# Kernel tuning notes

Hardware: AMD Instinct MI355X
Metric: run time of the kernel (lower is better)

## Reference

```python
import jax, jax.numpy as jnp
import numpy as np

D_MODEL = 768
N_HEAD = 12
N_KV_HEADS = 4
HEAD_DIM = D_MODEL // N_HEAD
N_REPEAT = N_HEAD // N_KV_HEADS
ROPE_BASE = 10000.0


def _rotate_half(x):
    # Faithful to the torch impl: reshape(..., 2, d/2) -> transpose(-2,-1) -> reshape
    # (interleaves the two halves), then chunk and cat(-x2, x1).
    d = x.shape[-1]
    xh = x.reshape(*x.shape[:-1], 2, d // 2).swapaxes(-2, -1).reshape(x.shape)
    x1, x2 = jnp.split(xh, 2, axis=-1)
    return jnp.concatenate([-x2, x1], axis=-1)


def _rope(x, pos):
    # x: [B, h, T, d], pos: [T] int
    d = x.shape[-1]
    inv_freq = 1.0 / (ROPE_BASE ** (jnp.arange(0, d, 2, dtype=jnp.float32) / d))
    freqs = pos.astype(jnp.float32)[:, None] * inv_freq[None, :]      # [T, d/2]
    emb = jnp.concatenate([freqs, freqs], axis=-1)                     # [T, d]
    cos = jnp.cos(emb)[None, None]                                     # [1,1,T,d]
    sin = jnp.sin(emb)[None, None]
    xf = x.astype(jnp.float32)
    return (xf * cos + _rotate_half(xf) * sin).astype(x.dtype)


def setup_inputs() -> dict:
    key = jax.random.key(0)
    ks = jax.random.split(key, 6)
    B, T, C = 8, 1024, D_MODEL
    s = 0.02
    return {
        "x": jax.random.normal(ks[0], (B, T, C), dtype=jnp.float32),
        "pos": jnp.arange(T, dtype=jnp.int32),
        "q_w": jax.random.normal(ks[1], (C, N_HEAD * HEAD_DIM), dtype=jnp.float32) * s,
        "q_b": jnp.zeros((N_HEAD * HEAD_DIM,), dtype=jnp.float32),
        "k_w": jax.random.normal(ks[2], (C, N_KV_HEADS * HEAD_DIM), dtype=jnp.float32) * s,
        "k_b": jnp.zeros((N_KV_HEADS * HEAD_DIM,), dtype=jnp.float32),
        "v_w": jax.random.normal(ks[3], (C, N_KV_HEADS * HEAD_DIM), dtype=jnp.float32) * s,
        "v_b": jnp.zeros((N_KV_HEADS * HEAD_DIM,), dtype=jnp.float32),
        "o_w": jax.random.normal(ks[4], (C, C), dtype=jnp.float32) * s,
        "o_b": jnp.zeros((C,), dtype=jnp.float32),
    }


def reference(x, pos, q_w, q_b, k_w, k_b, v_w, v_b, o_w, o_b):
    B, T, C = x.shape
    hd, H, KVH, rep = HEAD_DIM, N_HEAD, N_KV_HEADS, N_REPEAT

    Q = (x @ q_w + q_b).reshape(B, T, H, hd).transpose(0, 2, 1, 3)     # [B,H,T,hd]
    K = (x @ k_w + k_b).reshape(B, T, KVH, hd).transpose(0, 2, 1, 3)   # [B,KVH,T,hd]
    V = (x @ v_w + v_b).reshape(B, T, KVH, hd).transpose(0, 2, 1, 3)

    Q = _rope(Q, pos)
    K = _rope(K, pos)

    # Grouped attention: avoid materializing repeated KV (equiv. to repeat_interleave).
    Qg = Q.reshape(B, KVH, rep, T, hd)
    scores = jnp.einsum("bgrtd,bgsd->bgrts", Qg, K) / np.sqrt(hd).astype(np.float32)
    causal = jnp.tril(jnp.ones((T, T), dtype=bool))
    scores = jnp.where(causal, scores, jnp.finfo(scores.dtype).min)
    probs = jax.nn.softmax(scores, axis=-1)
    out = jnp.einsum("bgrts,bgsd->bgrtd", probs, V)                    # [B,KVH,rep,T,hd]
    out = out.reshape(B, H, T, hd).transpose(0, 2, 1, 3).reshape(B, T, C)
    return out @ o_w + o_b
```

## Files before the change

kernel.cpp:

```cpp
#include <hip/hip_runtime.h>
#include <hip/hip_bf16.h>
#include <math.h>

#define BATCH 8
#define SEQ   1024
#define DM    768
#define NHEAD 12
#define KVH   4
#define HD    64
#define REP   3

#define QSCALE 0.18033688011112042f

typedef unsigned short u16;
typedef __attribute__((ext_vector_type(8))) __bf16 bf16x8;
typedef __attribute__((ext_vector_type(4))) float f32x4;
typedef __attribute__((ext_vector_type(4))) unsigned int u32x4;
typedef __attribute__((address_space(1))) const unsigned int gu32_c;
typedef __attribute__((address_space(3))) unsigned int su32;

__device__ __forceinline__ u16 f2bf(float f) {
    unsigned int u = __float_as_uint(f);
    u += 0x7fffu + ((u >> 16) & 1u);
    return (u16)(u >> 16);
}

__global__ __launch_bounds__(256) void cvt_all(
    const float* __restrict__ x,
    const float* __restrict__ qw, const float* __restrict__ kw,
    const float* __restrict__ vw, const float* __restrict__ ow,
    u16* __restrict__ xb, u16* __restrict__ wqkvt, u16* __restrict__ wot)
{
    const int NX = 8192 * DM / 4;
    const int NW = 1280 * DM;
    const int NO = DM * DM;
    const int i = blockIdx.x * 256 + threadIdx.x;
    if (i < NX) {
        const float4 v = ((const float4*)x)[i];
        ushort4 r;
        r.x = f2bf(v.x); r.y = f2bf(v.y); r.z = f2bf(v.z); r.w = f2bf(v.w);
        ((ushort4*)xb)[i] = r;
    } else if (i < NX + NW) {
        const int idx = i - NX;
        const int k = idx % DM;
        const int n = idx / DM;
        float v;
        if (n < 768)       v = qw[(size_t)k * 768 + n] * QSCALE;
        else if (n < 1024) v = kw[(size_t)k * 256 + (n - 768)];
        else               v = vw[(size_t)k * 256 + (n - 1024)];
        wqkvt[idx] = f2bf(v);
    } else if (i < NX + NW + NO) {
        const int idx = i - NX - NW;
        const int k = idx % DM;
        const int n = idx / DM;
        wot[idx] = f2bf(ow[(size_t)k * DM + n]);
    }
}

__device__ __forceinline__ void gemm128_body(
    const u16* __restrict__ A, const u16* __restrict__ B,
    int m0, int n0, u16 (*As)[4096], u16 (*Bs)[4096], f32x4 acc[4][4])
{
    const int tid  = threadIdx.x;
    const int lane = tid & 63;
    const int wid  = tid >> 6;
    const int wr = wid >> 1, wc = wid & 1;
    const int lo = lane & 15, hi = lane >> 4;

    const f32x4 z = {0.f, 0.f, 0.f, 0.f};
    #pragma unroll
    for (int i = 0; i < 4; i++)
        #pragma unroll
        for (int j = 0; j < 4; j++)
            acc[i][j] = z;

    const int NT = DM / 32;

    #define STAGE_G(kt_, sl_) do {                                            \
        _Pragma("unroll")                                                     \
        for (int r_ = 0; r_ < 2; ++r_) {                                      \
            const int idx_  = r_ * 256 + tid;                                 \
            const int row_  = idx_ >> 2;                                      \
            const int col_  = (idx_ & 3) << 3;                                \
            const int base_ = (r_ * 256 + wid * 64) * 8;                      \
            __builtin_amdgcn_global_load_lds(                                 \
                (gu32_c*)&A[(size_t)(m0 + row_) * DM + (kt_) * 32 + col_],    \
                (su32*)&As[sl_][base_], 16, 0, 0);                            \
            __builtin_amdgcn_global_load_lds(                                 \
                (gu32_c*)&B[(size_t)(n0 + row_) * DM + (kt_) * 32 + col_],    \
                (su32*)&Bs[sl_][base_], 16, 0, 0);                            \
        }                                                                     \
    } while (0)

    STAGE_G(0, 0);
    STAGE_G(1, 1);

    for (int kt = 0; kt < NT; ++kt) {
        const int k2 = (kt + 2 < NT) ? kt + 2 : NT - 1;
        STAGE_G(k2, (kt + 2) & 3);
        asm volatile("s_waitcnt vmcnt(8)" ::: "memory");
        __builtin_amdgcn_s_barrier();
        __builtin_amdgcn_sched_barrier(0);

        const int sl = kt & 3;
        bf16x8 af[4], bfr[4];
        #pragma unroll
        for (int i = 0; i < 4; i++) af[i]  = *(const bf16x8*)&As[sl][(wr * 64 + i * 16 + lo) * 32 + hi * 8];
        #pragma unroll
        for (int j = 0; j < 4; j++) bfr[j] = *(const bf16x8*)&Bs[sl][(wc * 64 + j * 16 + lo) * 32 + hi * 8];
        #pragma unroll
        for (int i = 0; i < 4; i++)
            #pragma unroll
            for (int j = 0; j < 4; j++)
                acc[i][j] = __builtin_amdgcn_mfma_f32_16x16x32_bf16(af[i], bfr[j], acc[i][j], 0, 0, 0);
    }
    #undef STAGE_G
}

__global__ __launch_bounds__(256) void gemm_qkv(
    const u16* __restrict__ xb, const u16* __restrict__ wt,
    const float* __restrict__ qb, const float* __restrict__ kb,
    const float* __restrict__ vb,
    u16* __restrict__ Q, u16* __restrict__ K, u16* __restrict__ Vr)
{
    __shared__ __align__(16) u16 As[4][4096];
    __shared__ __align__(16) u16 Bs[4][4096];
    const int id = (blockIdx.x & 7) * 80 + (blockIdx.x >> 3);
    const int m0 = (id / 10) * 128;
    const int n0 = (id % 10) * 128;
    f32x4 acc[4][4];
    gemm128_body(xb, wt, m0, n0, As, Bs, acc);

    const int tid = threadIdx.x;
    const int lane = tid & 63, wid = tid >> 6;
    const int wr = wid >> 1, wc = wid & 1;
    const int lo = lane & 15, hi = lane >> 4;

    #pragma unroll
    for (int j = 0; j < 4; j++) {
        const int n = n0 + wc * 64 + j * 16 + lo;
        u16* outp; int nl, Hcnt; float bias;
        if (n < 768)       { outp = Q;  nl = n;        Hcnt = NHEAD; bias = qb[n] * QSCALE; }
        else if (n < 1024) { outp = K;  nl = n - 768;  Hcnt = KVH;   bias = kb[nl]; }
        else               { outp = Vr; nl = n - 1024; Hcnt = KVH;   bias = vb[nl]; }
        const int head = nl >> 6, d = nl & 63;
        #pragma unroll
        for (int i = 0; i < 4; i++) {
            #pragma unroll
            for (int r = 0; r < 4; r++) {
                const int m = m0 + wr * 64 + i * 16 + hi * 4 + r;
                const int b = m >> 10, t = m & 1023;
                outp[(((size_t)(b * Hcnt + head)) * SEQ + t) * HD + d] =
                    f2bf(acc[i][j][r] + bias);
            }
        }
    }
}

__global__ __launch_bounds__(256) void vtrans_k(
    const u16* __restrict__ in, u16* __restrict__ out)
{
    __shared__ u16 T[64][72];
    const int blk = blockIdx.x;
    const int bg  = blk >> 4;
    const int t0  = (blk & 15) << 6;
    const int tid = threadIdx.x;
    const int tl  = tid & 63;
    const int d0  = (tid >> 6) << 4;

    union { u32x4 v[2]; u16 u[16]; } ld;
    const u16* src = in + ((size_t)bg * SEQ + t0 + tl) * HD + d0;
    ld.v[0] = *(const u32x4*)(src);
    ld.v[1] = *(const u32x4*)(src + 8);
    #pragma unroll
    for (int k = 0; k < 16; ++k) T[d0 + k][tl] = ld.u[k];
    __syncthreads();

    const int d  = tid >> 2;
    const int tc = (tid & 3) << 4;
    u16* dst = out + ((size_t)bg * HD + d) * SEQ + t0 + tc;
    *(u32x4*)(dst)     = *(const u32x4*)&T[d][tc];
    *(u32x4*)(dst + 8) = *(const u32x4*)&T[d][tc + 8];
}

__global__ __launch_bounds__(256) void gemm_oproj(
    const u16* __restrict__ Ab, const u16* __restrict__ wt,
    const float* __restrict__ ob, float* __restrict__ outp)
{
    __shared__ __align__(16) u16 As[4][4096];
    __shared__ __align__(16) u16 Bs[4][4096];
    const int id = (blockIdx.x & 7) * 48 + (blockIdx.x >> 3);
    const int m0 = (id / 6) * 128;
    const int n0 = (id % 6) * 128;
    f32x4 acc[4][4];
    gemm128_body(Ab, wt, m0, n0, As, Bs, acc);

    const int tid = threadIdx.x;
    const int lane = tid & 63, wid = tid >> 6;
    const int wr = wid >> 1, wc = wid & 1;
    const int lo = lane & 15, hi = lane >> 4;

    #pragma unroll
    for (int j = 0; j < 4; j++) {
        const int n = n0 + wc * 64 + j * 16 + lo;
        const float bias = ob[n];
        #pragma unroll
        for (int i = 0; i < 4; i++) {
            #pragma unroll
            for (int r = 0; r < 4; r++) {
                const int m = m0 + wr * 64 + i * 16 + hi * 4 + r;
                outp[(size_t)m * DM + n] = acc[i][j][r] + bias;
            }
        }
    }
}

__global__ __launch_bounds__(256) void rope_naive(
    const __hip_bfloat16* __restrict__ Qin, __hip_bfloat16* __restrict__ Qout,
    const __hip_bfloat16* __restrict__ Kin, __hip_bfloat16* __restrict__ Kout,
    const int* __restrict__ pos)
{
    const long long qrows = (long long)BATCH * NHEAD * SEQ;
    const long long krows = (long long)BATCH * KVH * SEQ;
    const long long gid = (long long)blockIdx.x * 256 + threadIdx.x;
    if (gid >= (qrows + krows) * 64) return;
    long long row = gid >> 6;
    const int j = (int)(gid & 63);
    const __hip_bfloat16* in; __hip_bfloat16* outb;
    if (row < qrows) { in = Qin; outb = Qout; }
    else             { in = Kin; outb = Kout; row -= qrows; }
    const int t = (int)(row & (SEQ - 1));

    float p;
    if (pos[1] == 1)                              p = (float)pos[t];
    else if (((const float*)pos)[1] == 1.0f)      p = ((const float*)pos)[t];
    else                                          p = (float)pos[2 * t];

    const float inv = exp2f(-(float)(j & 31) * (13.287712379549449f / 32.0f));
    float sv, cv;
    sincosf(p * inv, &sv, &cv);
    const int partner = (j & 1) * 32 + (j >> 1) + ((j < 32) ? 16 : -16);
    const float sign  = (j < 32) ? -1.0f : 1.0f;
    const float val  = __bfloat162float(in[row * HD + j]);
    const float pv   = __bfloat162float(in[row * HD + partner]);
    outb[row * HD + j] = __float2bfloat16(val * cv + sign * pv * sv);
}

__device__ __forceinline__ void strip_compute(
    const bf16x8& qf0, const bf16x8& qf1,
    const bf16x8& k0, const bf16x8& k1, const bf16x8& k2, const bf16x8& k3,
    const bf16x8* vv, bool diag, int msk0, int hi,
    float& m, float& l, f32x4* O)
{
    const f32x4 z = {0.f, 0.f, 0.f, 0.f};
    f32x4 a0 = z, a1 = z;
    __builtin_amdgcn_s_setprio(1);
    a0 = __builtin_amdgcn_mfma_f32_16x16x32_bf16(k0, qf0, a0, 0, 0, 0);
    a0 = __builtin_amdgcn_mfma_f32_16x16x32_bf16(k1, qf1, a0, 0, 0, 0);
    a1 = __builtin_amdgcn_mfma_f32_16x16x32_bf16(k2, qf0, a1, 0, 0, 0);
    a1 = __builtin_amdgcn_mfma_f32_16x16x32_bf16(k3, qf1, a1, 0, 0, 0);
    __builtin_amdgcn_s_setprio(0);

    float sc[8];
    #pragma unroll
    for (int e = 0; e < 8; ++e)
        sc[e] = (e < 4) ? a0[e & 3] : a1[e & 3];
    if (diag) {
        #pragma unroll
        for (int e = 0; e < 8; ++e) {
            const int srel = ((e >> 2) << 4) + (hi << 2) + (e & 3);
            if (srel > msk0) sc[e] = -3.0e38f;
        }
    }
    float pm = sc[0];
    #pragma unroll
    for (int e = 1; e < 8; ++e) pm = fmaxf(pm, sc[e]);

    if (!__all(pm - m <= 8.0f)) {
        float pr = fmaxf(pm, __shfl_xor(pm, 16));
        pr = fmaxf(pr, __shfl_xor(pr, 32));
        const float mn = fmaxf(m, pr);
        const float f = exp2f(m - mn);
        l *= f;
        #pragma unroll
        for (int r = 0; r < 4; ++r) {
            const float fr = __shfl(f, hi * 4 + r);
            #pragma unroll
            for (int dj = 0; dj < 4; ++dj) O[dj][r] *= fr;
        }
        m = mn;
    }

    union { u16 u[8]; bf16x8 v; } pu;
    float ps = 0.f;
    #pragma unroll
    for (int e = 0; e < 8; ++e) {
        const float p = exp2f(sc[e] - m);
        ps += p;
        pu.u[e] = f2bf(p);
    }
    l += ps;

    __builtin_amdgcn_s_setprio(1);
    #pragma unroll
    for (int dj = 0; dj < 4; ++dj)
        O[dj] = __builtin_amdgcn_mfma_f32_16x16x32_bf16(pu.v, vv[dj], O[dj], 0, 0, 0);
    __builtin_amdgcn_s_setprio(0);
}

__global__ __launch_bounds__(256, 4) void attn_mfma(
    const u16* __restrict__ Q, const u16* __restrict__ K,
    const u16* __restrict__ Vt, u16* __restrict__ outp)
{
    __shared__ __align__(16) u16 Ks[4][2048];
    __shared__ __align__(16) u16 Vs[4][2048];

    const int blk = blockIdx.x;
    const int xcd = blk & 7;
    const int jj  = blk >> 3;
    const int bg  = (xcd << 2) + (jj & 3);
    const int rh  = jj >> 2;
    const int a   = 15 - rh / 3;
    const int hl  = rh % 3;
    const int b   = bg >> 2, g = bg & 3;
    const int h   = g * REP + hl;

    const int wid  = threadIdx.x >> 6;
    const int lane = threadIdx.x & 63;
    const int lo = lane & 15, hi = lane >> 4;

    const int w    = (a << 2) + wid;
    const int q0   = w << 4;
    const int dT   = w >> 1;
    const int msk0 = lo + ((w & 1) << 4);
    const int nstT = (a << 1) + 2;

    const u16* Kp = K  + (size_t)(b * KVH + g) * SEQ * HD;
    const u16* Vp = Vt + (size_t)(b * KVH + g) * SEQ * HD;

    const int jK = (wid << 6) + lane;
    const int sKoff = (jK ^ ((jK >> 3) & 7)) << 3;
    int vsoff[4];
    #pragma unroll
    for (int q = 0; q < 4; ++q) {
        const int dw  = (wid << 8) + (q << 6) + lane;
        const int R   = dw >> 4;
        const int wd  = dw & 15;
        const int hpl = (wd >> 2) ^ ((R >> 1) & 3);
        vsoff[q] = (R << 10) + (hpl << 2) + (((wd >> 1) & 1) << 4) + ((wd & 1) << 1);
    }

    const u16* Qp = Q + ((size_t)(b * NHEAD + h) * SEQ + q0) * HD;
    const bf16x8 qf0 = *(const bf16x8*)&Qp[(size_t)lo * HD + hi * 8];
    const bf16x8 qf1 = *(const bf16x8*)&Qp[(size_t)lo * HD + 32 + hi * 8];

    const f32x4 z = {0.f, 0.f, 0.f, 0.f};
    f32x4 O[4];
    #pragma unroll
    for (int dj = 0; dj < 4; ++dj) O[dj] = z;
    float m = -3.0e38f, l = 0.f;

    #define STAGE(st_, sl_) do {                                              \
        const int s0_ = (st_) << 5;                                           \
        __builtin_amdgcn_global_load_lds(                                     \
            (gu32_c*)(Kp + (s0_ << 6) + sKoff),                               \
            (su32*)&Ks[sl_][wid << 9], 16, 0, 0);                             \
        _Pragma("unroll")                                                     \
        for (int q_ = 0; q_ < 4; ++q_)                                        \
            __builtin_amdgcn_global_load_lds(                                 \
                (gu32_c*)(Vp + s0_ + vsoff[q_]),                              \
                (su32*)&Vs[sl_][(wid << 9) + (q_ << 7)], 4, 0, 0);            \
    } while (0)

    STAGE(0, 0);
    STAGE(1, 1);

    const int xorK = lo & 7;
    for (int st = 0; st < nstT; ++st) {
        const int s2 = (st + 2 < nstT) ? st + 2 : nstT - 1;
        STAGE(s2, (st + 2) & 3);
        asm volatile("s_waitcnt vmcnt(10)" ::: "memory");
        __builtin_amdgcn_s_barrier();
        __builtin_amdgcn_sched_barrier(0);

        if (st <= dT) {
            const int sl = st & 3;
            const u16* kb_ = Ks[sl];
            const bf16x8 k0 = *(const bf16x8*)&kb_[((lo << 3) + (hi ^ xorK)) << 3];
            const bf16x8 k1 = *(const bf16x8*)&kb_[((lo << 3) + ((4 + hi) ^ xorK)) << 3];
            const bf16x8 k2 = *(const bf16x8*)&kb_[(((16 + lo) << 3) + (hi ^ xorK)) << 3];
            const bf16x8 k3 = *(const bf16x8*)&kb_[(((16 + lo) << 3) + ((4 + hi) ^ xorK)) << 3];
            bf16x8 vv[4];
            #pragma unroll
            for (int dj = 0; dj < 4; ++dj) {
                const int R = dj * 16 + lo;
                vv[dj] = *(const bf16x8*)&Vs[sl][(R << 5) + ((hi ^ ((R >> 1) & 3)) << 3)];
            }
            strip_compute(qf0, qf1, k0, k1, k2, k3, vv, st == dT, msk0, hi, m, l, O);
        }
    }
    #undef STAGE

    l += __shfl_xor(l, 16); l += __shfl_xor(l, 32);
    #pragma unroll
    for (int r = 0; r < 4; ++r) {
        const float li = 1.0f / fmaxf(__shfl(l, hi * 4 + r), 1e-37f);
        const int t = q0 + hi * 4 + r;
        #pragma unroll
        for (int dj = 0; dj < 4; ++dj)
            outp[((size_t)(b * SEQ + t)) * DM + h * HD + dj * 16 + lo] = f2bf(O[dj][r] * li);
    }
}

extern "C" void kernel_launch(void* const* d_in, const int* in_sizes, int n_in,
                              void* d_out, int out_size, void* d_ws, size_t ws_size,
                              hipStream_t stream) {
    const float* x   = (const float*)d_in[0];
    const int*   pos = (const int*)d_in[1];
    const float* qw  = (const float*)d_in[2];
    const float* qb  = (const float*)d_in[3];
    const float* kw  = (const float*)d_in[4];
    const float* kb  = (const float*)d_in[5];
    const float* vw  = (const float*)d_in[6];
    const float* vb  = (const float*)d_in[7];
    const float* ow  = (const float*)d_in[8];
    const float* ob  = (const float*)d_in[9];
    float* out = (float*)d_out;

    u16* xb    = (u16*)d_ws;
    u16* Wqkvt = xb    + (size_t)8192 * DM;
    u16* Wot   = Wqkvt + (size_t)1280 * DM;
    u16* Qbuf  = Wot   + (size_t)DM * DM;
    u16* Kbuf  = Qbuf  + (size_t)BATCH * NHEAD * SEQ * HD;
    u16* Krot  = Kbuf  + (size_t)BATCH * KVH * SEQ * HD;
    u16* Vtb   = Krot  + (size_t)BATCH * KVH * SEQ * HD;
    u16* Qrot  = xb;
    u16* attn  = Qbuf;
    u16* Vraw  = Krot;

    const int NCVT = 8192 * DM / 4 + 1280 * DM + DM * DM;
    cvt_all<<<(NCVT + 255) / 256, 256, 0, stream>>>(x, qw, kw, vw, ow, xb, Wqkvt, Wot);

    gemm_qkv<<<640, 256, 0, stream>>>(xb, Wqkvt, qb, kb, vb, Qbuf, Kbuf, Vraw);

    vtrans_k<<<512, 256, 0, stream>>>(Vraw, Vtb);

    const long long allrows = (long long)BATCH * (NHEAD + KVH) * SEQ;
    rope_naive<<<(int)((allrows * 64 + 255) / 256), 256, 0, stream>>>(
        (const __hip_bfloat16*)Qbuf, (__hip_bfloat16*)Qrot,
        (const __hip_bfloat16*)Kbuf, (__hip_bfloat16*)Krot, pos);

    attn_mfma<<<1536, 256, 0, stream>>>(Qrot, Krot, Vtb, attn);

    gemm_oproj<<<384, 256, 0, stream>>>(attn, Wot, ob, out);
}
```

Before: 215.1 us.

## Shrink GEMM M-tile to 64 and fuse V transpose into QKV epilogue

```diff
diff --git a/kernel.cpp b/kernel.cpp
--- a/kernel.cpp
+++ b/kernel.cpp
@@ -57,9 +57,9 @@
     }
 }
 
-__device__ __forceinline__ void gemm128_body(
+__device__ __forceinline__ void gemm64_body(
     const u16* __restrict__ A, const u16* __restrict__ B,
-    int m0, int n0, u16 (*As)[4096], u16 (*Bs)[4096], f32x4 acc[4][4])
+    int m0, int n0, u16 (*As)[2048], u16 (*Bs)[4096], f32x4 acc[2][4])
 {
     const int tid  = threadIdx.x;
     const int lane = tid & 63;
@@ -69,14 +69,19 @@
 
     const f32x4 z = {0.f, 0.f, 0.f, 0.f};
     #pragma unroll
-    for (int i = 0; i < 4; i++)
+    for (int i = 0; i < 2; i++)
         #pragma unroll
         for (int j = 0; j < 4; j++)
             acc[i][j] = z;
 
     const int NT = DM / 32;
+    const int rowA = tid >> 2;
+    const int colA = (tid & 3) << 3;
 
     #define STAGE_G(kt_, sl_) do {                                            \
+        __builtin_amdgcn_global_load_lds(                                     \
+            (gu32_c*)&A[(size_t)(m0 + rowA) * DM + (kt_) * 32 + colA],        \
+            (su32*)&As[sl_][wid << 9], 16, 0, 0);                             \
         _Pragma("unroll")                                                     \
         for (int r_ = 0; r_ < 2; ++r_) {                                      \
             const int idx_  = r_ * 256 + tid;                                 \
@@ -84,9 +89,6 @@
             const int col_  = (idx_ & 3) << 3;                                \
             const int base_ = (r_ * 256 + wid * 64) * 8;                      \
             __builtin_amdgcn_global_load_lds(                                 \
-                (gu32_c*)&A[(size_t)(m0 + row_) * DM + (kt_) * 32 + col_],    \
-                (su32*)&As[sl_][base_], 16, 0, 0);                            \
-            __builtin_amdgcn_global_load_lds(                                 \
                 (gu32_c*)&B[(size_t)(n0 + row_) * DM + (kt_) * 32 + col_],    \
                 (su32*)&Bs[sl_][base_], 16, 0, 0);                            \
         }                                                                     \
@@ -98,18 +100,18 @@
     for (int kt = 0; kt < NT; ++kt) {
         const int k2 = (kt + 2 < NT) ? kt + 2 : NT - 1;
         STAGE_G(k2, (kt + 2) & 3);
-        asm volatile("s_waitcnt vmcnt(8)" ::: "memory");
+        asm volatile("s_waitcnt vmcnt(6)" ::: "memory");
         __builtin_amdgcn_s_barrier();
         __builtin_amdgcn_sched_barrier(0);
 
         const int sl = kt & 3;
-        bf16x8 af[4], bfr[4];
-        #pragma unroll
-        for (int i = 0; i < 4; i++) af[i]  = *(const bf16x8*)&As[sl][(wr * 64 + i * 16 + lo) * 32 + hi * 8];
+        bf16x8 af[2], bfr[4];
+        #pragma unroll
+        for (int i = 0; i < 2; i++) af[i]  = *(const bf16x8*)&As[sl][(wr * 32 + i * 16 + lo) * 32 + hi * 8];
         #pragma unroll
         for (int j = 0; j < 4; j++) bfr[j] = *(const bf16x8*)&Bs[sl][(wc * 64 + j * 16 + lo) * 32 + hi * 8];
         #pragma unroll
-        for (int i = 0; i < 4; i++)
+        for (int i = 0; i < 2; i++)
             #pragma unroll
             for (int j = 0; j < 4; j++)
                 acc[i][j] = __builtin_amdgcn_mfma_f32_16x16x32_bf16(af[i], bfr[j], acc[i][j], 0, 0, 0);
@@ -117,19 +119,19 @@
     #undef STAGE_G
 }
 
-__global__ __launch_bounds__(256) void gemm_qkv(
+__global__ __launch_bounds__(256, 2) void gemm_qkv(
     const u16* __restrict__ xb, const u16* __restrict__ wt,
     const float* __restrict__ qb, const float* __restrict__ kb,
     const float* __restrict__ vb,
-    u16* __restrict__ Q, u16* __restrict__ K, u16* __restrict__ Vr)
-{
-    __shared__ __align__(16) u16 As[4][4096];
+    u16* __restrict__ Q, u16* __restrict__ K, u16* __restrict__ Vt)
+{
+    __shared__ __align__(16) u16 As[4][2048];
     __shared__ __align__(16) u16 Bs[4][4096];
-    const int id = (blockIdx.x & 7) * 80 + (blockIdx.x >> 3);
-    const int m0 = (id / 10) * 128;
+    const int id = (blockIdx.x & 7) * 160 + (blockIdx.x >> 3);
+    const int m0 = (id / 10) * 64;
     const int n0 = (id % 10) * 128;
-    f32x4 acc[4][4];
-    gemm128_body(xb, wt, m0, n0, As, Bs, acc);
+    f32x4 acc[2][4];
+    gemm64_body(xb, wt, m0, n0, As, Bs, acc);
 
     const int tid = threadIdx.x;
     const int lane = tid & 63, wid = tid >> 6;
@@ -139,61 +141,51 @@
     #pragma unroll
     for (int j = 0; j < 4; j++) {
         const int n = n0 + wc * 64 + j * 16 + lo;
-        u16* outp; int nl, Hcnt; float bias;
-        if (n < 768)       { outp = Q;  nl = n;        Hcnt = NHEAD; bias = qb[n] * QSCALE; }
-        else if (n < 1024) { outp = K;  nl = n - 768;  Hcnt = KVH;   bias = kb[nl]; }
-        else               { outp = Vr; nl = n - 1024; Hcnt = KVH;   bias = vb[nl]; }
-        const int head = nl >> 6, d = nl & 63;
-        #pragma unroll
-        for (int i = 0; i < 4; i++) {
-            #pragma unroll
-            for (int r = 0; r < 4; r++) {
-                const int m = m0 + wr * 64 + i * 16 + hi * 4 + r;
+        if (n < 1024) {
+            u16* outp; int nl, Hcnt; float bias;
+            if (n < 768) { outp = Q; nl = n;       Hcnt = NHEAD; bias = qb[n] * QSCALE; }
+            else         { outp = K; nl = n - 768; Hcnt = KVH;   bias = kb[nl]; }
+            const int head = nl >> 6, d = nl & 63;
+            #pragma unroll
+            for (int i = 0; i < 2; i++) {
+                #pragma unroll
+                for (int r = 0; r < 4; r++) {
+                    const int m = m0 + wr * 32 + i * 16 + hi * 4 + r;
+                    const int b = m >> 10, t = m & 1023;
+                    outp[(((size_t)(b * Hcnt + head)) * SEQ + t) * HD + d] =
+                        f2bf(acc[i][j][r] + bias);
+                }
+            }
+        } else {
+            const int nl = n - 1024;
+            const float bias = vb[nl];
+            const int head = nl >> 6, d = nl & 63;
+            #pragma unroll
+            for (int i = 0; i < 2; i++) {
+                ushort4 vs;
+                vs.x = f2bf(acc[i][j][0] + bias);
+                vs.y = f2bf(acc[i][j][1] + bias);
+                vs.z = f2bf(acc[i][j][2] + bias);
+                vs.w = f2bf(acc[i][j][3] + bias);
+                const int m = m0 + wr * 32 + i * 16 + hi * 4;
                 const int b = m >> 10, t = m & 1023;
-                outp[(((size_t)(b * Hcnt + head)) * SEQ + t) * HD + d] =
-                    f2bf(acc[i][j][r] + bias);
+                *(ushort4*)&Vt[(((size_t)(b * KVH + head)) * HD + d) * SEQ + t] = vs;
             }
         }
     }
 }
 
-__global__ __launch_bounds__(256) void vtrans_k(
-    const u16* __restrict__ in, u16* __restrict__ out)
-{
-    __shared__ u16 T[64][72];
-    const int blk = blockIdx.x;
-    const int bg  = blk >> 4;
-    const int t0  = (blk & 15) << 6;
-    const int tid = threadIdx.x;
-    const int tl  = tid & 63;
-    const int d0  = (tid >> 6) << 4;
-
-    union { u32x4 v[2]; u16 u[16]; } ld;
-    const u16* src = in + ((size_t)bg * SEQ + t0 + tl) * HD + d0;
-    ld.v[0] = *(const u32x4*)(src);
-    ld.v[1] = *(const u32x4*)(src + 8);
-    #pragma unroll
-    for (int k = 0; k < 16; ++k) T[d0 + k][tl] = ld.u[k];
-    __syncthreads();
-
-    const int d  = tid >> 2;
-    const int tc = (tid & 3) << 4;
-    u16* dst = out + ((size_t)bg * HD + d) * SEQ + t0 + tc;
-    *(u32x4*)(dst)     = *(const u32x4*)&T[d][tc];
-    *(u32x4*)(dst + 8) = *(const u32x4*)&T[d][tc + 8];
-}
-
-__global__ __launch_bounds__(256) void gemm_oproj(
+__global__ __launch_bounds__(256, 2) void gemm_oproj(
     const u16* __restrict__ Ab, const u16* __restrict__ wt,
     const float* __restrict__ ob, float* __restrict__ outp)
 {
-    __shared__ __align__(16) u16 As[4][4096];
+    __shared__ __align__(16) u16 As[4][2048];
     __shared__ __align__(16) u16 Bs[4][4096];
-    const int id = (blockIdx.x & 7) * 48 + (blockIdx.x >> 3);
-    const int m0 = (id / 6) * 128;
+    const int id = (blockIdx.x & 7) * 96 + (blockIdx.x >> 3);
+    const int m0 = (id / 6) * 64;
     const int n0 = (id % 6) * 128;
-    f32x4 acc[4][4];
-    gemm128_body(Ab, wt, m0, n0, As, Bs, acc);
+    f32x4 acc[2][4];
+    gemm64_body(Ab, wt, m0, n0, As, Bs, acc);
 
     const int tid = threadIdx.x;
     const int lane = tid & 63, wid = tid >> 6;
@@ -205,10 +197,10 @@
         const int n = n0 + wc * 64 + j * 16 + lo;
         const float bias = ob[n];
         #pragma unroll
-        for (int i = 0; i < 4; i++) {
+        for (int i = 0; i < 2; i++) {
             #pragma unroll
             for (int r = 0; r < 4; r++) {
-                const int m = m0 + wr * 64 + i * 16 + hi * 4 + r;
+                const int m = m0 + wr * 32 + i * 16 + hi * 4 + r;
                 outp[(size_t)m * DM + n] = acc[i][j][r] + bias;
             }
         }
@@ -436,14 +428,11 @@
     u16* Vtb   = Krot  + (size_t)BATCH * KVH * SEQ * HD;
     u16* Qrot  = xb;
     u16* attn  = Qbuf;
-    u16* Vraw  = Krot;
 
     const int NCVT = 8192 * DM / 4 + 1280 * DM + DM * DM;
     cvt_all<<<(NCVT + 255) / 256, 256, 0, stream>>>(x, qw, kw, vw, ow, xb, Wqkvt, Wot);
 
-    gemm_qkv<<<640, 256, 0, stream>>>(xb, Wqkvt, qb, kb, vb, Qbuf, Kbuf, Vraw);
-
-    vtrans_k<<<512, 256, 0, stream>>>(Vraw, Vtb);
+    gemm_qkv<<<1280, 256, 0, stream>>>(xb, Wqkvt, qb, kb, vb, Qbuf, Kbuf, Vtb);
 
     const long long allrows = (long long)BATCH * (NHEAD + KVH) * SEQ;
     rope_naive<<<(int)((allrows * 64 + 255) / 256), 256, 0, stream>>>(
@@ -452,5 +441,5 @@
 
     attn_mfma<<<1536, 256, 0, stream>>>(Qrot, Krot, Vtb, attn);
 
-    gemm_oproj<<<384, 256, 0, stream>>>(attn, Wot, ob, out);
-}
+    gemm_oproj<<<768, 256, 0, stream>>>(attn, Wot, ob, out);
+}
```

Result: no change. 215.8 us (+0.3%).
